# Kernel tuning notes

Measured on AMD Instinct MI355X. Metric: run time of the kernel, lower is better.

Reference implementation:

```python
import jax, jax.numpy as jnp
import numpy as np

B, C_IN, H, W = 16, 16, 256, 256  # B must equal out_channels for the module's broadcast
C_OUT = 16


def setup_inputs() -> dict:
    key = jax.random.key(0)
    k1, k2, k3, k4 = jax.random.split(key, 4)
    return {
        "x_real": jax.random.normal(k1, (B, C_IN, H, W), dtype=jnp.float32),
        "x_imag": jax.random.normal(k2, (B, C_IN, H, W), dtype=jnp.float32),
        "w_real": jax.random.normal(k3, (C_OUT, C_IN, H, W), dtype=jnp.float32),
        "w_imag": jax.random.normal(k4, (C_OUT, C_IN, H, W), dtype=jnp.float32),
    }


def reference(x_real, x_imag, w_real, w_imag):
    # HolographicConv: ifft2(fft2(x) * W).real with complex x and W.
    x = jax.lax.complex(x_real, x_imag)            # (B, C_in, H, W) complex64
    w = jax.lax.complex(w_real, w_imag)            # (C_out, C_in, H, W) complex64
    x_freq = jnp.fft.fft2(x, axes=(-2, -1))
    conv_freq = x_freq * w                          # broadcast: B == C_out, k == H == W
    out = jnp.fft.ifft2(conv_freq, axes=(-2, -1))
    return out.real.astype(jnp.float32)
```

## Files before the change

kernel.cpp:

```cpp
#include <hip/hip_runtime.h>


#define PI_F 3.14159265358979323846f

__device__ __forceinline__ float2 cadd(float2 a, float2 b){ return make_float2(a.x+b.x, a.y+b.y); }
__device__ __forceinline__ float2 csub(float2 a, float2 b){ return make_float2(a.x-b.x, a.y-b.y); }
__device__ __forceinline__ float2 cmul(float2 a, float2 b){
  return make_float2(a.x*b.x - a.y*b.y, a.x*b.y + a.y*b.x);
}

__device__ __forceinline__ int SW(int e){ return e ^ (e >> 4); }

template<int DIR>
__device__ __forceinline__ void bfly4(float2& a, float2& b, float2& c, float2& d,
                                      float2 w1, float2 w2, float2 w3)
{
  float2 apc = cadd(a,c), amc = csub(a,c);
  float2 bpd = cadd(b,d), bmd = csub(b,d);
  float2 jb = (DIR > 0) ? make_float2(-bmd.y, bmd.x)
                        : make_float2( bmd.y,-bmd.x);
  a = cadd(apc, bpd);
  b = cmul(w1, csub(amc, jb));
  c = cmul(w2, csub(apc, bpd));
  d = cmul(w3, cadd(amc, jb));
}

template<int DIR>
__device__ __forceinline__ void fft256(float2 v[4], float2* scr, const float2* tw, int lane)
{
  #pragma unroll
  for (int st = 0; st < 3; ++st) {
    const int s  = 1 << (2*st);
    const int ps = lane & ~(s-1);
    const int q  = lane &  (s-1);
    float2 w1 = tw[ps];
    float2 w2 = tw[(2*ps) & 255];
    float2 w3 = tw[(3*ps) & 255];
    if (DIR < 0) { w1.y = -w1.y; w2.y = -w2.y; w3.y = -w3.y; }
    bfly4<DIR>(v[0], v[1], v[2], v[3], w1, w2, w3);
    const int dbase = q + 4*ps;
    __builtin_amdgcn_wave_barrier();
    scr[SW(dbase + 0*s)] = v[0];
    scr[SW(dbase + 1*s)] = v[1];
    scr[SW(dbase + 2*s)] = v[2];
    scr[SW(dbase + 3*s)] = v[3];
    __builtin_amdgcn_wave_barrier();
    v[0] = scr[SW(lane +   0)];
    v[1] = scr[SW(lane +  64)];
    v[2] = scr[SW(lane + 128)];
    v[3] = scr[SW(lane + 192)];
    __builtin_amdgcn_wave_barrier();
  }
  const float2 one = make_float2(1.f, 0.f);
  bfly4<DIR>(v[0], v[1], v[2], v[3], one, one, one);
}

__device__ __forceinline__ void init_tw(float2* tw, int tid)
{
  float sv, cv;
  sincosf(-2.0f * PI_F * (float)tid / 256.0f, &sv, &cv);
  tw[tid] = make_float2(cv, sv);
}

__global__ __launch_bounds__(256) void k_rowfft(const float* __restrict__ xr,
                                                const float* __restrict__ xi,
                                                float2* __restrict__ ws)
{
  __shared__ float2 tw[256];
  __shared__ float2 scr[4][256];
  const int tid = threadIdx.x;
  init_tw(tw, tid);
  __syncthreads();
  const int wave = tid >> 6, lane = tid & 63;
  const long long row = (long long)blockIdx.x * 4 + wave;
  const float* pr = xr + row * 256;
  const float* pi = xi + row * 256;
  float2 v[4];
  #pragma unroll
  for (int r = 0; r < 4; ++r)
    v[r] = make_float2(pr[lane + 64*r], pi[lane + 64*r]);
  fft256<1>(v, scr[wave], tw, lane);
  float2* o = ws + row * 256;
  #pragma unroll
  for (int r = 0; r < 4; ++r) o[lane + 64*r] = v[r];
}

__global__ __launch_bounds__(256) void k_colpass(float2* __restrict__ ws,
                                                 const float* __restrict__ wr,
                                                 const float* __restrict__ wi,
                                                 int img0)
{
  __shared__ float2 xt[256][17];
  __shared__ float2 wt[256][17];
  __shared__ float2 scr[4][256];
  __shared__ float2 tw[256];
  const int tid = threadIdx.x;
  init_tw(tw, tid);
  const int imgl = blockIdx.x >> 4;
  const int w0   = (blockIdx.x & 15) * 16;
  const size_t base_l = (size_t)imgl * 65536 + w0;
  const size_t base_g = (size_t)(img0 + imgl) * 65536 + w0;
  const int c  = tid & 15;
  const int h0 = tid >> 4;
  #pragma unroll
  for (int t = 0; t < 16; ++t) {
    const int h = h0 + t*16;
    xt[h][c] = ws[base_l + (size_t)h*256 + c];
    wt[h][c] = make_float2(wr[base_g + (size_t)h*256 + c],
                           wi[base_g + (size_t)h*256 + c]);
  }
  __syncthreads();
  const int wave = tid >> 6, lane = tid & 63;
  #pragma unroll 1
  for (int cc = 0; cc < 4; ++cc) {
    const int col = wave * 4 + cc;
    float2 v[4];
    #pragma unroll
    for (int r = 0; r < 4; ++r) v[r] = xt[lane + 64*r][col];
    fft256<1>(v, scr[wave], tw, lane);
    #pragma unroll
    for (int r = 0; r < 4; ++r) v[r] = cmul(v[r], wt[lane + 64*r][col]);
    fft256<-1>(v, scr[wave], tw, lane);
    #pragma unroll
    for (int r = 0; r < 4; ++r) xt[lane + 64*r][col] = v[r];
  }
  __syncthreads();
  #pragma unroll
  for (int t = 0; t < 16; ++t) {
    const int h = h0 + t*16;
    ws[base_l + (size_t)h*256 + c] = xt[h][c];
  }
}

__global__ __launch_bounds__(256) void k_rowifft(const float2* __restrict__ ws,
                                                 float* __restrict__ out)
{
  __shared__ float2 tw[256];
  __shared__ float2 scr[4][256];
  const int tid = threadIdx.x;
  init_tw(tw, tid);
  __syncthreads();
  const int wave = tid >> 6, lane = tid & 63;
  const long long row = (long long)blockIdx.x * 4 + wave;
  const float2* p = ws + row * 256;
  float2 v[4];
  #pragma unroll
  for (int r = 0; r < 4; ++r) v[r] = p[lane + 64*r];
  fft256<-1>(v, scr[wave], tw, lane);
  float* o = out + row * 256;
  const float sc = 1.0f / 65536.0f;
  #pragma unroll
  for (int r = 0; r < 4; ++r) o[lane + 64*r] = v[r].x * sc;
}

extern "C" void kernel_launch(void* const* d_in, const int* in_sizes, int n_in,
                              void* d_out, int out_size, void* d_ws, size_t ws_size,
                              hipStream_t stream)
{
  const float* xr = (const float*)d_in[0];
  const float* xi = (const float*)d_in[1];
  const float* wr = (const float*)d_in[2];
  const float* wi = (const float*)d_in[3];
  float* out = (float*)d_out;

  const int IMG = 256;
  const size_t per_img = (size_t)65536 * sizeof(float2);
  int ipc = (int)(ws_size / per_img);
  if (ipc < 1)  ipc = 1;
  if (ipc > IMG) ipc = IMG;
  float2* wsp = (float2*)d_ws;

  for (int img0 = 0; img0 < IMG; img0 += ipc) {
    const int n = (IMG - img0 < ipc) ? (IMG - img0) : ipc;
    k_rowfft <<<dim3(n*64), dim3(256), 0, stream>>>(xr + (size_t)img0*65536,
                                                    xi + (size_t)img0*65536, wsp);
    k_colpass<<<dim3(n*16), dim3(256), 0, stream>>>(wsp, wr, wi, img0);
    k_rowifft<<<dim3(n*64), dim3(256), 0, stream>>>(wsp, out + (size_t)img0*65536);
  }
}
```

Baseline: 174.5 us.

## Swap FFT axis order with transposed workspace and batch two FFTs per wave

The column FFT now runs first on the inputs and writes a transposed workspace. The middle pass then does row FFT, the weight multiply and the inverse row FFT, reading the weights as contiguous rows instead of staging them as strided tiles in shared memory. The final inverse column pass transposes back through shared memory before storing. Each wave now interleaves two independent 256-point FFTs for more ILP, and launch bounds request 3 blocks per CU. Shared memory per block drops in the middle pass, but every kernel now does strided tile loads or stores.

```diff
diff --git a/kernel.cpp b/kernel.cpp
--- a/kernel.cpp
+++ b/kernel.cpp
@@ -26,7 +26,9 @@
 }
 
 template<int DIR>
-__device__ __forceinline__ void fft256(float2 v[4], float2* scr, const float2* tw, int lane)
+__device__ __forceinline__ void fft256_x2(float2 va[4], float2 vb[4],
+                                          float2* sa, float2* sb,
+                                          const float2* tw, int lane)
 {
   #pragma unroll
   for (int st = 0; st < 3; ++st) {
@@ -37,22 +39,32 @@
     float2 w2 = tw[(2*ps) & 255];
     float2 w3 = tw[(3*ps) & 255];
     if (DIR < 0) { w1.y = -w1.y; w2.y = -w2.y; w3.y = -w3.y; }
-    bfly4<DIR>(v[0], v[1], v[2], v[3], w1, w2, w3);
+    bfly4<DIR>(va[0], va[1], va[2], va[3], w1, w2, w3);
+    bfly4<DIR>(vb[0], vb[1], vb[2], vb[3], w1, w2, w3);
     const int dbase = q + 4*ps;
     __builtin_amdgcn_wave_barrier();
-    scr[SW(dbase + 0*s)] = v[0];
-    scr[SW(dbase + 1*s)] = v[1];
-    scr[SW(dbase + 2*s)] = v[2];
-    scr[SW(dbase + 3*s)] = v[3];
+    sa[SW(dbase + 0*s)] = va[0];
+    sb[SW(dbase + 0*s)] = vb[0];
+    sa[SW(dbase + 1*s)] = va[1];
+    sb[SW(dbase + 1*s)] = vb[1];
+    sa[SW(dbase + 2*s)] = va[2];
+    sb[SW(dbase + 2*s)] = vb[2];
+    sa[SW(dbase + 3*s)] = va[3];
+    sb[SW(dbase + 3*s)] = vb[3];
     __builtin_amdgcn_wave_barrier();
-    v[0] = scr[SW(lane +   0)];
-    v[1] = scr[SW(lane +  64)];
-    v[2] = scr[SW(lane + 128)];
-    v[3] = scr[SW(lane + 192)];
+    va[0] = sa[SW(lane +   0)];
+    vb[0] = sb[SW(lane +   0)];
+    va[1] = sa[SW(lane +  64)];
+    vb[1] = sb[SW(lane +  64)];
+    va[2] = sa[SW(lane + 128)];
+    vb[2] = sb[SW(lane + 128)];
+    va[3] = sa[SW(lane + 192)];
+    vb[3] = sb[SW(lane + 192)];
     __builtin_amdgcn_wave_barrier();
   }
   const float2 one = make_float2(1.f, 0.f);
-  bfly4<DIR>(v[0], v[1], v[2], v[3], one, one, one);
+  bfly4<DIR>(va[0], va[1], va[2], va[3], one, one, one);
+  bfly4<DIR>(vb[0], vb[1], vb[2], vb[3], one, one, one);
 }
 
 __device__ __forceinline__ void init_tw(float2* tw, int tid)
@@ -62,95 +74,134 @@
   tw[tid] = make_float2(cv, sv);
 }
 
-__global__ __launch_bounds__(256) void k_rowfft(const float* __restrict__ xr,
-                                                const float* __restrict__ xi,
-                                                float2* __restrict__ ws)
-{
-  __shared__ float2 tw[256];
-  __shared__ float2 scr[4][256];
-  const int tid = threadIdx.x;
-  init_tw(tw, tid);
-  __syncthreads();
-  const int wave = tid >> 6, lane = tid & 63;
-  const long long row = (long long)blockIdx.x * 4 + wave;
-  const float* pr = xr + row * 256;
-  const float* pi = xi + row * 256;
-  float2 v[4];
-  #pragma unroll
-  for (int r = 0; r < 4; ++r)
-    v[r] = make_float2(pr[lane + 64*r], pi[lane + 64*r]);
-  fft256<1>(v, scr[wave], tw, lane);
-  float2* o = ws + row * 256;
-  #pragma unroll
-  for (int r = 0; r < 4; ++r) o[lane + 64*r] = v[r];
-}
-
-__global__ __launch_bounds__(256) void k_colpass(float2* __restrict__ ws,
-                                                 const float* __restrict__ wr,
-                                                 const float* __restrict__ wi,
-                                                 int img0)
+__global__ __launch_bounds__(256, 3) void k_colfft(const float* __restrict__ xr,
+                                                   const float* __restrict__ xi,
+                                                   float2* __restrict__ wsT)
 {
   __shared__ float2 xt[256][17];
-  __shared__ float2 wt[256][17];
-  __shared__ float2 scr[4][256];
+  __shared__ float2 scr[4][2][256];
   __shared__ float2 tw[256];
   const int tid = threadIdx.x;
   init_tw(tw, tid);
   const int imgl = blockIdx.x >> 4;
-  const int w0   = (blockIdx.x & 15) * 16;
-  const size_t base_l = (size_t)imgl * 65536 + w0;
-  const size_t base_g = (size_t)(img0 + imgl) * 65536 + w0;
+  const int v0   = (blockIdx.x & 15) * 16;
+  const size_t ib = (size_t)imgl * 65536;
   const int c  = tid & 15;
   const int h0 = tid >> 4;
   #pragma unroll
   for (int t = 0; t < 16; ++t) {
-    const int h = h0 + t*16;
-    xt[h][c] = ws[base_l + (size_t)h*256 + c];
-    wt[h][c] = make_float2(wr[base_g + (size_t)h*256 + c],
-                           wi[base_g + (size_t)h*256 + c]);
+    const int u = t*16 + h0;
+    xt[u][c] = make_float2(xr[ib + (size_t)u*256 + v0 + c],
+                           xi[ib + (size_t)u*256 + v0 + c]);
   }
   __syncthreads();
   const int wave = tid >> 6, lane = tid & 63;
   #pragma unroll 1
-  for (int cc = 0; cc < 4; ++cc) {
-    const int col = wave * 4 + cc;
-    float2 v[4];
-    #pragma unroll
-    for (int r = 0; r < 4; ++r) v[r] = xt[lane + 64*r][col];
-    fft256<1>(v, scr[wave], tw, lane);
-    #pragma unroll
-    for (int r = 0; r < 4; ++r) v[r] = cmul(v[r], wt[lane + 64*r][col]);
-    fft256<-1>(v, scr[wave], tw, lane);
-    #pragma unroll
-    for (int r = 0; r < 4; ++r) xt[lane + 64*r][col] = v[r];
-  }
-  __syncthreads();
-  #pragma unroll
-  for (int t = 0; t < 16; ++t) {
-    const int h = h0 + t*16;
-    ws[base_l + (size_t)h*256 + c] = xt[h][c];
-  }
-}
-
-__global__ __launch_bounds__(256) void k_rowifft(const float2* __restrict__ ws,
-                                                 float* __restrict__ out)
-{
+  for (int cc = 0; cc < 2; ++cc) {
+    const int colA = wave*4 + cc*2, colB = colA + 1;
+    float2 va[4], vb[4];
+    #pragma unroll
+    for (int r = 0; r < 4; ++r) { va[r] = xt[lane + 64*r][colA];
+                                  vb[r] = xt[lane + 64*r][colB]; }
+    fft256_x2<1>(va, vb, scr[wave][0], scr[wave][1], tw, lane);
+    float2* oA = wsT + ib + (size_t)(v0 + colA)*256;
+    float2* oB = wsT + ib + (size_t)(v0 + colB)*256;
+    #pragma unroll
+    for (int r = 0; r < 4; ++r) { oA[lane + 64*r] = va[r];
+                                  oB[lane + 64*r] = vb[r]; }
+  }
+}
+
+__global__ __launch_bounds__(256, 3) void k_rowpass(float2* __restrict__ wsT,
+                                                    const float* __restrict__ wr,
+                                                    const float* __restrict__ wi,
+                                                    int img0)
+{
+  __shared__ float2 xt[256][17];
+  __shared__ float2 scr[4][2][256];
   __shared__ float2 tw[256];
-  __shared__ float2 scr[4][256];
   const int tid = threadIdx.x;
   init_tw(tw, tid);
+  const int imgl = blockIdx.x >> 4;
+  const int k0   = (blockIdx.x & 15) * 16;
+  const size_t ib = (size_t)imgl * 65536;
+  const size_t wb = (size_t)(img0 + imgl) * 65536;
+  const int c  = tid & 15;
+  const int h0 = tid >> 4;
+  #pragma unroll
+  for (int t = 0; t < 16; ++t) {
+    const int v = t*16 + h0;
+    xt[v][c] = wsT[ib + (size_t)v*256 + k0 + c];
+  }
   __syncthreads();
   const int wave = tid >> 6, lane = tid & 63;
-  const long long row = (long long)blockIdx.x * 4 + wave;
-  const float2* p = ws + row * 256;
-  float2 v[4];
-  #pragma unroll
-  for (int r = 0; r < 4; ++r) v[r] = p[lane + 64*r];
-  fft256<-1>(v, scr[wave], tw, lane);
-  float* o = out + row * 256;
+  #pragma unroll 1
+  for (int cc = 0; cc < 2; ++cc) {
+    const int colA = wave*4 + cc*2, colB = colA + 1;
+    float2 va[4], vb[4];
+    #pragma unroll
+    for (int r = 0; r < 4; ++r) { va[r] = xt[lane + 64*r][colA];
+                                  vb[r] = xt[lane + 64*r][colB]; }
+    fft256_x2<1>(va, vb, scr[wave][0], scr[wave][1], tw, lane);
+    const float* wrA = wr + wb + (size_t)(k0 + colA)*256;
+    const float* wiA = wi + wb + (size_t)(k0 + colA)*256;
+    const float* wrB = wr + wb + (size_t)(k0 + colB)*256;
+    const float* wiB = wi + wb + (size_t)(k0 + colB)*256;
+    #pragma unroll
+    for (int r = 0; r < 4; ++r) {
+      const int l = lane + 64*r;
+      va[r] = cmul(va[r], make_float2(wrA[l], wiA[l]));
+      vb[r] = cmul(vb[r], make_float2(wrB[l], wiB[l]));
+    }
+    fft256_x2<-1>(va, vb, scr[wave][0], scr[wave][1], tw, lane);
+    #pragma unroll
+    for (int r = 0; r < 4; ++r) { xt[lane + 64*r][colA] = va[r];
+                                  xt[lane + 64*r][colB] = vb[r]; }
+  }
+  __syncthreads();
+  #pragma unroll
+  for (int t = 0; t < 16; ++t) {
+    const int v = t*16 + h0;
+    wsT[ib + (size_t)v*256 + k0 + c] = xt[v][c];
+  }
+}
+
+__global__ __launch_bounds__(256, 3) void k_rowifft(const float2* __restrict__ wsT,
+                                                    float* __restrict__ out)
+{
+  __shared__ float ot[256][17];
+  __shared__ float2 scr[4][2][256];
+  __shared__ float2 tw[256];
+  const int tid = threadIdx.x;
+  init_tw(tw, tid);
+  __syncthreads();
+  const int imgl = blockIdx.x >> 4;
+  const int v0   = (blockIdx.x & 15) * 16;
+  const size_t ib = (size_t)imgl * 65536;
+  const int wave = tid >> 6, lane = tid & 63;
   const float sc = 1.0f / 65536.0f;
-  #pragma unroll
-  for (int r = 0; r < 4; ++r) o[lane + 64*r] = v[r].x * sc;
+  #pragma unroll 1
+  for (int cc = 0; cc < 2; ++cc) {
+    const int colA = wave*4 + cc*2, colB = colA + 1;
+    const float2* pA = wsT + ib + (size_t)(v0 + colA)*256;
+    const float2* pB = wsT + ib + (size_t)(v0 + colB)*256;
+    float2 va[4], vb[4];
+    #pragma unroll
+    for (int r = 0; r < 4; ++r) { va[r] = pA[lane + 64*r];
+                                  vb[r] = pB[lane + 64*r]; }
+    fft256_x2<-1>(va, vb, scr[wave][0], scr[wave][1], tw, lane);
+    #pragma unroll
+    for (int r = 0; r < 4; ++r) { ot[lane + 64*r][colA] = va[r].x * sc;
+                                  ot[lane + 64*r][colB] = vb[r].x * sc; }
+  }
+  __syncthreads();
+  const int c  = tid & 15;
+  const int h0 = tid >> 4;
+  #pragma unroll
+  for (int t = 0; t < 16; ++t) {
+    const int u = t*16 + h0;
+    out[ib + (size_t)u*256 + v0 + c] = ot[u][c];
+  }
 }
 
 extern "C" void kernel_launch(void* const* d_in, const int* in_sizes, int n_in,
@@ -166,15 +217,15 @@
   const int IMG = 256;
   const size_t per_img = (size_t)65536 * sizeof(float2);
   int ipc = (int)(ws_size / per_img);
-  if (ipc < 1)  ipc = 1;
+  if (ipc < 1)   ipc = 1;
   if (ipc > IMG) ipc = IMG;
   float2* wsp = (float2*)d_ws;
 
   for (int img0 = 0; img0 < IMG; img0 += ipc) {
     const int n = (IMG - img0 < ipc) ? (IMG - img0) : ipc;
-    k_rowfft <<<dim3(n*64), dim3(256), 0, stream>>>(xr + (size_t)img0*65536,
+    k_colfft <<<dim3(n*16), dim3(256), 0, stream>>>(xr + (size_t)img0*65536,
                                                     xi + (size_t)img0*65536, wsp);
-    k_colpass<<<dim3(n*16), dim3(256), 0, stream>>>(wsp, wr, wi, img0);
-    k_rowifft<<<dim3(n*64), dim3(256), 0, stream>>>(wsp, out + (size_t)img0*65536);
-  }
-}
+    k_rowpass<<<dim3(n*16), dim3(256), 0, stream>>>(wsp, wr, wi, img0);
+    k_rowifft<<<dim3(n*16), dim3(256), 0, stream>>>(wsp, out + (size_t)img0*65536);
+  }
+}
```

After: 180.6 us. 1.03x slower.
